# Kernel optimization log

Measured on AMD Instinct MI355X. Metric: run time of the kernel, lower is better.

Reference implementation:

```python
import jax, jax.numpy as jnp
import numpy as np

N_NODES = 100000


def gcn_conv(x, edge_index, W, b):
    """PyG-style GCNConv: add self-loops, symmetric deg^{-1/2} normalization,
    then scatter-sum of transformed source features into targets."""
    n = x.shape[0]
    loops = jnp.arange(n, dtype=edge_index.dtype)
    row = jnp.concatenate([edge_index[0], loops])  # source
    col = jnp.concatenate([edge_index[1], loops])  # target
    deg = jax.ops.segment_sum(jnp.ones_like(col, dtype=x.dtype), col, num_segments=n)
    dinv = jnp.where(deg > 0, jax.lax.rsqrt(deg), 0.0)
    norm = dinv[row] * dinv[col]  # [E+N]
    h = x @ W  # [N, out]
    msg = h[row] * norm[:, None]  # gather + scale, [E+N, out]
    out = jax.ops.segment_sum(msg, col, num_segments=n)
    return out + b


def setup_inputs() -> dict:
    key = jax.random.key(0)
    k1, k2, k3, k4, k5 = jax.random.split(key, 5)
    x = jax.random.normal(k1, (N_NODES, 972), dtype=jnp.float32)
    edge_index = jax.random.randint(k2, (2, 1600000), 0, N_NODES, dtype=jnp.int64)
    edge_label_index = jax.random.randint(k3, (2, 1000000), 0, N_NODES, dtype=jnp.int64)
    W1 = jax.random.normal(k4, (384, 128), dtype=jnp.float32) * (1.0 / np.sqrt(384))
    b1 = jnp.zeros((128,), dtype=jnp.float32)
    W2 = jax.random.normal(k5, (128, 64), dtype=jnp.float32) * (1.0 / np.sqrt(128))
    b2 = jnp.zeros((64,), dtype=jnp.float32)
    return {"x": x, "edge_index": edge_index, "edge_label_index": edge_label_index,
            "W1": W1, "b1": b1, "W2": W2, "b2": b2}


def reference(x, edge_index, edge_label_index, W1, b1, W2, b2):
    # encode: slice features, two GCN layers with relu between
    h = x[:, 588:]  # [N, 384]
    h = jax.nn.relu(gcn_conv(h, edge_index, W1, b1))
    z = gcn_conv(h, edge_index, W2, b2)  # [N, 64]
    # decode: gather-dot-sum over labeled edges
    logits = jnp.sum(z[edge_label_index[0]] * z[edge_label_index[1]], axis=-1)
    return logits
```

## Files before the change

kernel.cpp:

```cpp
#include <hip/hip_runtime.h>
#include <hip/hip_bf16.h>

#define N_NODES 100000
#define N_EDGES 1600000
#define N_LBL   1000000
#define XC 972
#define XO 588
#define D1 128
#define D2 64
#define GEMM1_BLOCKS ((N_NODES + 63) / 64)
#define PLACE_BLOCKS (N_EDGES / 256)

typedef float f32x4 __attribute__((ext_vector_type(4)));
typedef short bf16x8 __attribute__((ext_vector_type(8)));

__device__ inline unsigned f2bf(float f) {
    unsigned u = __float_as_uint(f);
    return (u + 0x7fffu + ((u >> 16) & 1u)) >> 16;
}
__device__ inline float bf_lo(unsigned v) { return __uint_as_float(v << 16); }
__device__ inline float bf_hi(unsigned v) { return __uint_as_float(v & 0xffff0000u); }

__device__ inline unsigned pack_bf2(float lo, float hi) {
    union { __hip_bfloat162 h; unsigned u; } p;
    p.h = __float22bfloat162_rn(make_float2(lo, hi));
    return p.u;
}
__device__ inline bf16x8 to_bf8(float4 a, float4 b) {
    union { __hip_bfloat162 h[4]; bf16x8 v; } u;
    u.h[0] = __float22bfloat162_rn(make_float2(a.x, a.y));
    u.h[1] = __float22bfloat162_rn(make_float2(a.z, a.w));
    u.h[2] = __float22bfloat162_rn(make_float2(b.x, b.y));
    u.h[3] = __float22bfloat162_rn(make_float2(b.z, b.w));
    return u.v;
}
__device__ inline void add8(float (&a)[8], uint4 u) {
    a[0] += bf_lo(u.x); a[1] += bf_hi(u.x);
    a[2] += bf_lo(u.y); a[3] += bf_hi(u.y);
    a[4] += bf_lo(u.z); a[5] += bf_hi(u.z);
    a[6] += bf_lo(u.w); a[7] += bf_hi(u.w);
}
__device__ inline void fma8(float (&a)[8], uint4 u, float s) {
    a[0] = fmaf(bf_lo(u.x), s, a[0]); a[1] = fmaf(bf_hi(u.x), s, a[1]);
    a[2] = fmaf(bf_lo(u.y), s, a[2]); a[3] = fmaf(bf_hi(u.y), s, a[3]);
    a[4] = fmaf(bf_lo(u.z), s, a[4]); a[5] = fmaf(bf_hi(u.z), s, a[5]);
    a[6] = fmaf(bf_lo(u.w), s, a[6]); a[7] = fmaf(bf_hi(u.w), s, a[7]);
}

__global__ __launch_bounds__(256) void k_prep(const float* __restrict__ W1,
                                              const float* __restrict__ W2,
                                              unsigned short* __restrict__ w1p,
                                              unsigned short* __restrict__ w2p,
                                              unsigned* __restrict__ cursor) {
    int i = blockIdx.x * 256 + threadIdx.x;
    if (i < N_NODES) cursor[i] = 0u;
    if (i < 49152) {
        int j = i & 7, lane = (i >> 3) & 63, nt = (i >> 9) & 7, ks = i >> 12;
        int k = ks * 32 + ((lane >> 4) << 3) + j;
        int n = (nt << 4) + (lane & 15);
        w1p[i] = (unsigned short)f2bf(W1[k * D1 + n]);
    } else if (i < 57344) {
        int t = i - 49152;
        int j = t & 7, lane = (t >> 3) & 63, nt = (t >> 9) & 3, ks = t >> 11;
        int k = ks * 32 + ((lane >> 4) << 3) + j;
        int n = (nt << 4) + (lane & 15);
        w2p[t] = (unsigned short)f2bf(W2[k * D2 + n]);
    }
}

__global__ __launch_bounds__(256) void k_mega(const float* __restrict__ x,
                                              const unsigned short* __restrict__ w1p,
                                              unsigned short* __restrict__ s1,
                                              const int* __restrict__ erow,
                                              const int* __restrict__ ecol,
                                              unsigned* __restrict__ cursor,
                                              int* __restrict__ srcidx) {
    if (blockIdx.x < GEMM1_BLOCKS) {
        const int lane = threadIdx.x & 63;
        const int wid  = threadIdx.x >> 6;
        const int lrow = lane & 15;
        const int kq   = lane >> 4;

        const int row0 = blockIdx.x * 64 + wid * 16;
        const int rc = min(row0 + lrow, N_NODES - 1);
        const float* pA = x + (size_t)rc * XC + XO + (kq << 3);

        f32x4 acc[8];
#pragma unroll
        for (int t = 0; t < 8; ++t) acc[t] = (f32x4)0.f;

#pragma unroll 2
        for (int ks = 0; ks < 12; ++ks) {
            float4 a0 = *reinterpret_cast<const float4*>(pA + ks * 32);
            float4 a1 = *reinterpret_cast<const float4*>(pA + ks * 32 + 4);
            bf16x8 aA = to_bf8(a0, a1);
#pragma unroll
            for (int t = 0; t < 8; ++t) {
                bf16x8 bf = *reinterpret_cast<const bf16x8*>(
                    w1p + ((size_t)((ks * 8 + t) * 64 + lane) << 3));
                acc[t] = __builtin_amdgcn_mfma_f32_16x16x32_bf16(aA, bf, acc[t], 0, 0, 0);
            }
        }

        const int rowq = row0 + kq * 4;
#pragma unroll
        for (int r = 0; r < 4; ++r) {
            int rw = rowq + r;
            if (rw < N_NODES) {
#pragma unroll
                for (int t = 0; t < 8; ++t)
                    s1[(size_t)rw * D1 + lrow + t * 16] =
                        (unsigned short)f2bf(acc[t][r]);
            }
        }
    } else {
        int e = (blockIdx.x - GEMM1_BLOCKS) * 256 + threadIdx.x;
        int c = ecol[e];
        unsigned j = atomicAdd(&cursor[c], 1u);
        srcidx[((size_t)c << 6) + j] = erow[e];
    }
}

__global__ __launch_bounds__(256) void k_fused(const unsigned short* __restrict__ s1,
                                               const int* __restrict__ srcidx,
                                               const unsigned* __restrict__ deg,
                                               const float* __restrict__ b1,
                                               const unsigned short* __restrict__ w2p,
                                               unsigned short* __restrict__ s2) {
    const int lane = threadIdx.x & 63;
    const int wid  = threadIdx.x >> 6;
    const int n    = lane & 15;
    const int kq   = lane >> 4;
    const int base = blockIdx.x * 64 + wid * 16;
    const int c  = base + n;
    const int cc = min(c, N_NODES - 1);

    const int cnt = (int)deg[cc];
    const float dc = rsqrtf((float)(cnt + 1));

    float acc[4][8];
#pragma unroll
    for (int p = 0; p < 4; ++p)
#pragma unroll
        for (int j = 0; j < 8; ++j) acc[p][j] = 0.f;

    {
        const unsigned short* srow = s1 + (size_t)cc * D1 + (kq << 3);
        fma8(acc[0], *reinterpret_cast<const uint4*>(srow),      dc);
        fma8(acc[1], *reinterpret_cast<const uint4*>(srow + 32), dc);
        fma8(acc[2], *reinterpret_cast<const uint4*>(srow + 64), dc);
        fma8(acc[3], *reinterpret_cast<const uint4*>(srow + 96), dc);
    }

    const int* sp = srcidx + ((size_t)cc << 6);
    int j = 0;
    for (; j + 4 <= cnt; j += 4) {
        int4 idx = *reinterpret_cast<const int4*>(sp + j);
        const unsigned short* p0 = s1 + (size_t)idx.x * D1 + (kq << 3);
        const unsigned short* p1 = s1 + (size_t)idx.y * D1 + (kq << 3);
        const unsigned short* p2 = s1 + (size_t)idx.z * D1 + (kq << 3);
        const unsigned short* p3 = s1 + (size_t)idx.w * D1 + (kq << 3);
        unsigned g0 = deg[idx.x], g1 = deg[idx.y], g2 = deg[idx.z], g3 = deg[idx.w];
        uint4 a0 = *reinterpret_cast<const uint4*>(p0);
        uint4 a1 = *reinterpret_cast<const uint4*>(p0 + 32);
        uint4 a2 = *reinterpret_cast<const uint4*>(p0 + 64);
        uint4 a3 = *reinterpret_cast<const uint4*>(p0 + 96);
        uint4 b0 = *reinterpret_cast<const uint4*>(p1);
        uint4 b1x = *reinterpret_cast<const uint4*>(p1 + 32);
        uint4 b2 = *reinterpret_cast<const uint4*>(p1 + 64);
        uint4 b3 = *reinterpret_cast<const uint4*>(p1 + 96);
        uint4 c0 = *reinterpret_cast<const uint4*>(p2);
        uint4 c1 = *reinterpret_cast<const uint4*>(p2 + 32);
        uint4 c2 = *reinterpret_cast<const uint4*>(p2 + 64);
        uint4 c3 = *reinterpret_cast<const uint4*>(p2 + 96);
        uint4 e0 = *reinterpret_cast<const uint4*>(p3);
        uint4 e1 = *reinterpret_cast<const uint4*>(p3 + 32);
        uint4 e2 = *reinterpret_cast<const uint4*>(p3 + 64);
        uint4 e3 = *reinterpret_cast<const uint4*>(p3 + 96);
        float d0 = rsqrtf((float)(g0 + 1u));
        float d1 = rsqrtf((float)(g1 + 1u));
        float d2 = rsqrtf((float)(g2 + 1u));
        float d3 = rsqrtf((float)(g3 + 1u));
        fma8(acc[0], a0, d0); fma8(acc[1], a1, d0);
        fma8(acc[2], a2, d0); fma8(acc[3], a3, d0);
        fma8(acc[0], b0, d1); fma8(acc[1], b1x, d1);
        fma8(acc[2], b2, d1); fma8(acc[3], b3, d1);
        fma8(acc[0], c0, d2); fma8(acc[1], c1, d2);
        fma8(acc[2], c2, d2); fma8(acc[3], c3, d2);
        fma8(acc[0], e0, d3); fma8(acc[1], e1, d3);
        fma8(acc[2], e2, d3); fma8(acc[3], e3, d3);
    }
    for (; j < cnt; ++j) {
        int r = sp[j];
        float dr = rsqrtf((float)(deg[r] + 1u));
        const unsigned short* rr = s1 + (size_t)r * D1 + (kq << 3);
        fma8(acc[0], *reinterpret_cast<const uint4*>(rr),      dr);
        fma8(acc[1], *reinterpret_cast<const uint4*>(rr + 32), dr);
        fma8(acc[2], *reinterpret_cast<const uint4*>(rr + 64), dr);
        fma8(acc[3], *reinterpret_cast<const uint4*>(rr + 96), dr);
    }

    bf16x8 af[4];
#pragma unroll
    for (int p = 0; p < 4; ++p) {
        const float* bp = b1 + p * 32 + (kq << 3);
        float4 ba = *reinterpret_cast<const float4*>(bp);
        float4 bb = *reinterpret_cast<const float4*>(bp + 4);
        float4 h0 = make_float4(fmaxf(fmaf(acc[p][0], dc, ba.x), 0.f),
                                fmaxf(fmaf(acc[p][1], dc, ba.y), 0.f),
                                fmaxf(fmaf(acc[p][2], dc, ba.z), 0.f),
                                fmaxf(fmaf(acc[p][3], dc, ba.w), 0.f));
        float4 h1 = make_float4(fmaxf(fmaf(acc[p][4], dc, bb.x), 0.f),
                                fmaxf(fmaf(acc[p][5], dc, bb.y), 0.f),
                                fmaxf(fmaf(acc[p][6], dc, bb.z), 0.f),
                                fmaxf(fmaf(acc[p][7], dc, bb.w), 0.f));
        af[p] = to_bf8(h0, h1);
    }

    f32x4 acc2[4];
#pragma unroll
    for (int nt = 0; nt < 4; ++nt) acc2[nt] = (f32x4)0.f;
#pragma unroll
    for (int ks = 0; ks < 4; ++ks)
#pragma unroll
        for (int nt = 0; nt < 4; ++nt) {
            bf16x8 bf = *reinterpret_cast<const bf16x8*>(
                w2p + ((size_t)((ks * 4 + nt) * 64 + lane) << 3));
            acc2[nt] = __builtin_amdgcn_mfma_f32_16x16x32_bf16(af[ks], bf, acc2[nt], 0, 0, 0);
        }

#pragma unroll
    for (int r = 0; r < 4; ++r) {
        int rw = base + kq * 4 + r;
        if (rw < N_NODES) {
            float dm = rsqrtf((float)(deg[rw] + 1u));
#pragma unroll
            for (int nt = 0; nt < 4; ++nt)
                s2[(size_t)rw * D2 + nt * 16 + n] =
                    (unsigned short)f2bf(acc2[nt][r] * dm);
        }
    }
}

__global__ __launch_bounds__(256) void k_gather2(const unsigned short* __restrict__ s2,
                                                 const int* __restrict__ srcidx,
                                                 const unsigned* __restrict__ deg,
                                                 const float* __restrict__ b,
                                                 uint4* __restrict__ zv) {
    const int c    = blockIdx.x * 32 + (threadIdx.x >> 3);
    const int l8   = threadIdx.x & 7;

    float a[8];
#pragma unroll
    for (int j = 0; j < 8; ++j) a[j] = 0.f;
    add8(a, *reinterpret_cast<const uint4*>(s2 + (size_t)c * D2 + (l8 << 3)));

    const int cnt = (int)deg[c];
    const int* sp = srcidx + ((size_t)c << 6);
    int j = 0;
    for (; j + 4 <= cnt; j += 4) {
        int4 idx = *reinterpret_cast<const int4*>(sp + j);
        uint4 u0 = *reinterpret_cast<const uint4*>(s2 + (size_t)idx.x * D2 + (l8 << 3));
        uint4 u1 = *reinterpret_cast<const uint4*>(s2 + (size_t)idx.y * D2 + (l8 << 3));
        uint4 u2 = *reinterpret_cast<const uint4*>(s2 + (size_t)idx.z * D2 + (l8 << 3));
        uint4 u3 = *reinterpret_cast<const uint4*>(s2 + (size_t)idx.w * D2 + (l8 << 3));
        add8(a, u0); add8(a, u1); add8(a, u2); add8(a, u3);
    }
    for (; j < cnt; ++j) {
        int r = sp[j];
        add8(a, *reinterpret_cast<const uint4*>(s2 + (size_t)r * D2 + (l8 << 3)));
    }
    const float d = rsqrtf((float)(cnt + 1));
    const float4 b0 = reinterpret_cast<const float4*>(b)[l8 * 2];
    const float4 b1v = reinterpret_cast<const float4*>(b)[l8 * 2 + 1];
    uint4 o;
    o.x = pack_bf2(fmaf(a[0], d, b0.x),  fmaf(a[1], d, b0.y));
    o.y = pack_bf2(fmaf(a[2], d, b0.z),  fmaf(a[3], d, b0.w));
    o.z = pack_bf2(fmaf(a[4], d, b1v.x), fmaf(a[5], d, b1v.y));
    o.w = pack_bf2(fmaf(a[6], d, b1v.z), fmaf(a[7], d, b1v.w));
    zv[(size_t)c * 8 + l8] = o;
}

__global__ __launch_bounds__(256) void k_score(const uint4* __restrict__ Z,
                                               const int* __restrict__ ea,
                                               const int* __restrict__ eb,
                                               float* __restrict__ out) {
    int tid = blockIdx.x * 256 + threadIdx.x;
    int p = tid >> 3;
    int l = tid & 7;
    int2 us = *reinterpret_cast<const int2*>(ea + 2 * p);
    int2 vs = *reinterpret_cast<const int2*>(eb + 2 * p);
    uint4 a0 = Z[(size_t)us.x * 8 + l];
    uint4 c0 = Z[(size_t)vs.x * 8 + l];
    uint4 a1 = Z[(size_t)us.y * 8 + l];
    uint4 c1 = Z[(size_t)vs.y * 8 + l];
    float p0 = bf_lo(a0.x) * bf_lo(c0.x) + bf_hi(a0.x) * bf_hi(c0.x)
             + bf_lo(a0.y) * bf_lo(c0.y) + bf_hi(a0.y) * bf_hi(c0.y)
             + bf_lo(a0.z) * bf_lo(c0.z) + bf_hi(a0.z) * bf_hi(c0.z)
             + bf_lo(a0.w) * bf_lo(c0.w) + bf_hi(a0.w) * bf_hi(c0.w);
    float p1 = bf_lo(a1.x) * bf_lo(c1.x) + bf_hi(a1.x) * bf_hi(c1.x)
             + bf_lo(a1.y) * bf_lo(c1.y) + bf_hi(a1.y) * bf_hi(c1.y)
             + bf_lo(a1.z) * bf_lo(c1.z) + bf_hi(a1.z) * bf_hi(c1.z)
             + bf_lo(a1.w) * bf_lo(c1.w) + bf_hi(a1.w) * bf_hi(c1.w);
    p0 += __shfl_down(p0, 4, 8);  p1 += __shfl_down(p1, 4, 8);
    p0 += __shfl_down(p0, 2, 8);  p1 += __shfl_down(p1, 2, 8);
    p0 += __shfl_down(p0, 1, 8);  p1 += __shfl_down(p1, 1, 8);
    if (l == 0) *reinterpret_cast<float2*>(out + 2 * p) = make_float2(p0, p1);
}

extern "C" void kernel_launch(void* const* d_in, const int* in_sizes, int n_in,
                              void* d_out, int out_size, void* d_ws, size_t ws_size,
                              hipStream_t stream) {
    const float* x   = (const float*)d_in[0];
    const int*   ei  = (const int*)d_in[1];
    const int*   eli = (const int*)d_in[2];
    const float* W1  = (const float*)d_in[3];
    const float* b1  = (const float*)d_in[4];
    const float* W2  = (const float*)d_in[5];
    const float* b2  = (const float*)d_in[6];
    float* out = (float*)d_out;

    char* ws = (char*)d_ws;
    unsigned*       cursor = (unsigned*)(ws + 0);
    unsigned short* w1p    = (unsigned short*)(ws + 400000);
    unsigned short* w2p    = (unsigned short*)(ws + 498304);
    int*            srcidx = (int*)(ws + 514688);
    unsigned short* s1     = (unsigned short*)(ws + 26114688);
    unsigned short* s2     = (unsigned short*)(ws + 51714688);
    unsigned short* z      = (unsigned short*)(ws + 64514688);

    k_prep   <<<392, 256, 0, stream>>>(W1, W2, w1p, w2p, cursor);
    k_mega   <<<GEMM1_BLOCKS + PLACE_BLOCKS, 256, 0, stream>>>(x, w1p, s1, ei,
                                                               ei + N_EDGES, cursor, srcidx);
    k_fused  <<<(N_NODES + 63) / 64, 256, 0, stream>>>(s1, srcidx, cursor, b1, w2p, s2);
    k_gather2<<<N_NODES / 32, 256, 0, stream>>>(s2, srcidx, cursor, b2, (uint4*)z);
    k_score  <<<(size_t)N_LBL * 8 / 2 / 256, 256, 0, stream>>>((const uint4*)z, eli,
                                                               eli + N_LBL, out);
}
```

Measured before the change: 271.3 us.

## Interleave GEMM and edge-placement blocks, widen per-thread work, prefetch gather indices

The fused GEMM/placement kernel now interleaves one GEMM block with two placement blocks, so the compute-bound and atomic-bound work runs together on the device. Each placement thread now handles two edges. k_fused prefetches the next group of neighbor indices one iteration ahead. k_gather2 gets an 8-wide unrolled loop to keep more loads in flight, and k_score processes four label pairs per thread with vectorized index loads and stores. The aim is more memory-level parallelism and better overlap, at the cost of higher register pressure and possibly lower occupancy.

```diff
diff --git a/kernel.cpp b/kernel.cpp
--- a/kernel.cpp
+++ b/kernel.cpp
@@ -9,7 +9,8 @@
 #define D1 128
 #define D2 64
 #define GEMM1_BLOCKS ((N_NODES + 63) / 64)
-#define PLACE_BLOCKS (N_EDGES / 256)
+#define PLACE_BLOCKS (N_EDGES / 512)
+#define MEGA_BLOCKS  (GEMM1_BLOCKS + PLACE_BLOCKS)
 
 typedef float f32x4 __attribute__((ext_vector_type(4)));
 typedef short bf16x8 __attribute__((ext_vector_type(8)));
@@ -45,6 +46,12 @@
     a[2] = fmaf(bf_lo(u.y), s, a[2]); a[3] = fmaf(bf_hi(u.y), s, a[3]);
     a[4] = fmaf(bf_lo(u.z), s, a[4]); a[5] = fmaf(bf_hi(u.z), s, a[5]);
     a[6] = fmaf(bf_lo(u.w), s, a[6]); a[7] = fmaf(bf_hi(u.w), s, a[7]);
+}
+__device__ inline float dot8(uint4 a, uint4 c) {
+    return bf_lo(a.x) * bf_lo(c.x) + bf_hi(a.x) * bf_hi(c.x)
+         + bf_lo(a.y) * bf_lo(c.y) + bf_hi(a.y) * bf_hi(c.y)
+         + bf_lo(a.z) * bf_lo(c.z) + bf_hi(a.z) * bf_hi(c.z)
+         + bf_lo(a.w) * bf_lo(c.w) + bf_hi(a.w) * bf_hi(c.w);
 }
 
 __global__ __launch_bounds__(256) void k_prep(const float* __restrict__ W1,
@@ -75,13 +82,15 @@
                                               const int* __restrict__ ecol,
                                               unsigned* __restrict__ cursor,
                                               int* __restrict__ srcidx) {
-    if (blockIdx.x < GEMM1_BLOCKS) {
+    const int bid = blockIdx.x;
+    const int g = bid / 3, r3 = bid % 3;
+    if (r3 == 0) {
         const int lane = threadIdx.x & 63;
         const int wid  = threadIdx.x >> 6;
         const int lrow = lane & 15;
         const int kq   = lane >> 4;
 
-        const int row0 = blockIdx.x * 64 + wid * 16;
+        const int row0 = g * 64 + wid * 16;
         const int rc = min(row0 + lrow, N_NODES - 1);
         const float* pA = x + (size_t)rc * XC + XO + (kq << 3);
 
@@ -114,10 +123,14 @@
             }
         }
     } else {
-        int e = (blockIdx.x - GEMM1_BLOCKS) * 256 + threadIdx.x;
-        int c = ecol[e];
-        unsigned j = atomicAdd(&cursor[c], 1u);
-        srcidx[((size_t)c << 6) + j] = erow[e];
+        int pb = bid - g - 1;
+        int pe = pb * 256 + threadIdx.x;
+        int2 rw = *reinterpret_cast<const int2*>(erow + 2 * pe);
+        int2 cl = *reinterpret_cast<const int2*>(ecol + 2 * pe);
+        unsigned j0 = atomicAdd(&cursor[cl.x], 1u);
+        srcidx[((size_t)cl.x << 6) + j0] = rw.x;
+        unsigned j1 = atomicAdd(&cursor[cl.y], 1u);
+        srcidx[((size_t)cl.y << 6) + j1] = rw.y;
     }
 }
 
@@ -154,13 +167,16 @@
 
     const int* sp = srcidx + ((size_t)cc << 6);
     int j = 0;
+    int4 idx;
+    if (cnt >= 4) idx = *reinterpret_cast<const int4*>(sp);
     for (; j + 4 <= cnt; j += 4) {
-        int4 idx = *reinterpret_cast<const int4*>(sp + j);
-        const unsigned short* p0 = s1 + (size_t)idx.x * D1 + (kq << 3);
-        const unsigned short* p1 = s1 + (size_t)idx.y * D1 + (kq << 3);
-        const unsigned short* p2 = s1 + (size_t)idx.z * D1 + (kq << 3);
-        const unsigned short* p3 = s1 + (size_t)idx.w * D1 + (kq << 3);
-        unsigned g0 = deg[idx.x], g1 = deg[idx.y], g2 = deg[idx.z], g3 = deg[idx.w];
+        int4 cur = idx;
+        if (j + 8 <= cnt) idx = *reinterpret_cast<const int4*>(sp + j + 4);
+        const unsigned short* p0 = s1 + (size_t)cur.x * D1 + (kq << 3);
+        const unsigned short* p1 = s1 + (size_t)cur.y * D1 + (kq << 3);
+        const unsigned short* p2 = s1 + (size_t)cur.z * D1 + (kq << 3);
+        const unsigned short* p3 = s1 + (size_t)cur.w * D1 + (kq << 3);
+        unsigned g0 = deg[cur.x], g1 = deg[cur.y], g2 = deg[cur.z], g3 = deg[cur.w];
         uint4 a0 = *reinterpret_cast<const uint4*>(p0);
         uint4 a1 = *reinterpret_cast<const uint4*>(p0 + 32);
         uint4 a2 = *reinterpret_cast<const uint4*>(p0 + 64);
@@ -258,6 +274,20 @@
     const int cnt = (int)deg[c];
     const int* sp = srcidx + ((size_t)c << 6);
     int j = 0;
+    for (; j + 8 <= cnt; j += 8) {
+        int4 i0 = *reinterpret_cast<const int4*>(sp + j);
+        int4 i1 = *reinterpret_cast<const int4*>(sp + j + 4);
+        uint4 u0 = *reinterpret_cast<const uint4*>(s2 + (size_t)i0.x * D2 + (l8 << 3));
+        uint4 u1 = *reinterpret_cast<const uint4*>(s2 + (size_t)i0.y * D2 + (l8 << 3));
+        uint4 u2 = *reinterpret_cast<const uint4*>(s2 + (size_t)i0.z * D2 + (l8 << 3));
+        uint4 u3 = *reinterpret_cast<const uint4*>(s2 + (size_t)i0.w * D2 + (l8 << 3));
+        uint4 u4 = *reinterpret_cast<const uint4*>(s2 + (size_t)i1.x * D2 + (l8 << 3));
+        uint4 u5 = *reinterpret_cast<const uint4*>(s2 + (size_t)i1.y * D2 + (l8 << 3));
+        uint4 u6 = *reinterpret_cast<const uint4*>(s2 + (size_t)i1.z * D2 + (l8 << 3));
+        uint4 u7 = *reinterpret_cast<const uint4*>(s2 + (size_t)i1.w * D2 + (l8 << 3));
+        add8(a, u0); add8(a, u1); add8(a, u2); add8(a, u3);
+        add8(a, u4); add8(a, u5); add8(a, u6); add8(a, u7);
+    }
     for (; j + 4 <= cnt; j += 4) {
         int4 idx = *reinterpret_cast<const int4*>(sp + j);
         uint4 u0 = *reinterpret_cast<const uint4*>(s2 + (size_t)idx.x * D2 + (l8 << 3));
@@ -288,24 +318,29 @@
     int tid = blockIdx.x * 256 + threadIdx.x;
     int p = tid >> 3;
     int l = tid & 7;
-    int2 us = *reinterpret_cast<const int2*>(ea + 2 * p);
-    int2 vs = *reinterpret_cast<const int2*>(eb + 2 * p);
+    if (p >= N_LBL / 4) return;
+    int4 us = *reinterpret_cast<const int4*>(ea + 4 * p);
+    int4 vs = *reinterpret_cast<const int4*>(eb + 4 * p);
     uint4 a0 = Z[(size_t)us.x * 8 + l];
     uint4 c0 = Z[(size_t)vs.x * 8 + l];
     uint4 a1 = Z[(size_t)us.y * 8 + l];
     uint4 c1 = Z[(size_t)vs.y * 8 + l];
-    float p0 = bf_lo(a0.x) * bf_lo(c0.x) + bf_hi(a0.x) * bf_hi(c0.x)
-             + bf_lo(a0.y) * bf_lo(c0.y) + bf_hi(a0.y) * bf_hi(c0.y)
-             + bf_lo(a0.z) * bf_lo(c0.z) + bf_hi(a0.z) * bf_hi(c0.z)
-             + bf_lo(a0.w) * bf_lo(c0.w) + bf_hi(a0.w) * bf_hi(c0.w);
-    float p1 = bf_lo(a1.x) * bf_lo(c1.x) + bf_hi(a1.x) * bf_hi(c1.x)
-             + bf_lo(a1.y) * bf_lo(c1.y) + bf_hi(a1.y) * bf_hi(c1.y)
-             + bf_lo(a1.z) * bf_lo(c1.z) + bf_hi(a1.z) * bf_hi(c1.z)
-             + bf_lo(a1.w) * bf_lo(c1.w) + bf_hi(a1.w) * bf_hi(c1.w);
+    uint4 a2 = Z[(size_t)us.z * 8 + l];
+    uint4 c2 = Z[(size_t)vs.z * 8 + l];
+    uint4 a3 = Z[(size_t)us.w * 8 + l];
+    uint4 c3 = Z[(size_t)vs.w * 8 + l];
+    float p0 = dot8(a0, c0);
+    float p1 = dot8(a1, c1);
+    float p2 = dot8(a2, c2);
+    float p3 = dot8(a3, c3);
     p0 += __shfl_down(p0, 4, 8);  p1 += __shfl_down(p1, 4, 8);
+    p2 += __shfl_down(p2, 4, 8);  p3 += __shfl_down(p3, 4, 8);
     p0 += __shfl_down(p0, 2, 8);  p1 += __shfl_down(p1, 2, 8);
+    p2 += __shfl_down(p2, 2, 8);  p3 += __shfl_down(p3, 2, 8);
     p0 += __shfl_down(p0, 1, 8);  p1 += __shfl_down(p1, 1, 8);
-    if (l == 0) *reinterpret_cast<float2*>(out + 2 * p) = make_float2(p0, p1);
+    p2 += __shfl_down(p2, 1, 8);  p3 += __shfl_down(p3, 1, 8);
+    if (l == 0)
+        *reinterpret_cast<float4*>(out + 4 * p) = make_float4(p0, p1, p2, p3);
 }
 
 extern "C" void kernel_launch(void* const* d_in, const int* in_sizes, int n_in,
@@ -330,10 +365,10 @@
     unsigned short* z      = (unsigned short*)(ws + 64514688);
 
     k_prep   <<<392, 256, 0, stream>>>(W1, W2, w1p, w2p, cursor);
-    k_mega   <<<GEMM1_BLOCKS + PLACE_BLOCKS, 256, 0, stream>>>(x, w1p, s1, ei,
-                                                               ei + N_EDGES, cursor, srcidx);
+    k_mega   <<<MEGA_BLOCKS, 256, 0, stream>>>(x, w1p, s1, ei, ei + N_EDGES,
+                                               cursor, srcidx);
     k_fused  <<<(N_NODES + 63) / 64, 256, 0, stream>>>(s1, srcidx, cursor, b1, w2p, s2);
     k_gather2<<<N_NODES / 32, 256, 0, stream>>>(s2, srcidx, cursor, b2, (uint4*)z);
-    k_score  <<<(size_t)N_LBL * 8 / 2 / 256, 256, 0, stream>>>((const uint4*)z, eli,
+    k_score  <<<(N_LBL / 4 * 8 + 255) / 256, 256, 0, stream>>>((const uint4*)z, eli,
                                                                eli + N_LBL, out);
 }
```

Result: slower. 290.9 us (+7.2%).
